# Performance work log

Measured on AMD Instinct MI355X. Metric: run time of the kernel, lower is better.

## Reference

```python
import jax, jax.numpy as jnp
import numpy as np

N_SIDE = 30            # n lines per axis -> 900 primitives
GRID = 64              # grid_size
MAX_ELEMS = 32         # max_elements_per_cell
IMG = 2048             # render resolution -> 4.19M query points


def setup_inputs() -> dict:
    # Replicate the module's line-primitive initialization (one short line per n x n cell).
    rng = np.random.default_rng(42)
    n = N_SIDE
    cell_w = 1.0 / n
    ii, jj = np.meshgrid(np.arange(n), np.arange(n), indexing='ij')
    cx = (ii + 0.5) / n + (rng.random((n, n)) - 0.5) * 0.2 * cell_w
    cy = (jj + 0.5) / n + (rng.random((n, n)) - 0.5) * 0.2 * cell_w
    ang = rng.random((n, n)) * 2.0 * np.pi
    L = 0.3 * cell_w
    dx = np.cos(ang) * L
    dy = np.sin(ang) * L
    x0 = np.clip(cx - dx, 0.0, 1.0); y0 = np.clip(cy - dy, 0.0, 1.0)
    x1 = np.clip(cx + dx, 0.0, 1.0); y1 = np.clip(cy + dy, 0.0, 1.0)
    w = 0.6 / n
    # control points layout per line block: [x0, y0, x1, y1, width, 0]
    control = np.stack([x0, y0, x1, y1, np.full((n, n), w), np.zeros((n, n))], -1)
    control = control.reshape(-1, 6).astype(np.float32)
    widths = np.full((n * n,), w, np.float32)          # stroke_widths (block[7])
    colors = rng.random((n * n, 3)).astype(np.float32)  # fill_colors
    opac = np.ones((n * n,), np.float32)                # opacities
    bg = np.zeros((3,), np.float32)                     # background_color
    key = jax.random.key(0)
    x = jax.random.uniform(key, (IMG * IMG, 2), dtype=jnp.float32)
    return {
        'x': x,
        'control_points': jnp.asarray(control),
        'stroke_widths': jnp.asarray(widths),
        'fill_colors': jnp.asarray(colors),
        'opacities': jnp.asarray(opac),
        'background_color': jnp.asarray(bg),
    }


def _build_grid(control_points, stroke_widths, G, M):
    """Scatter-build: per grid cell, list of primitive indices whose (width-expanded)
    AABB overlaps the cell, plus a count (slot-0 count in the original kernel)."""
    x0, y0, x1, y1 = control_points[:, 0], control_points[:, 1], control_points[:, 2], control_points[:, 3]
    w = stroke_widths
    xmin = jnp.minimum(x0, x1) - w; xmax = jnp.maximum(x0, x1) + w
    ymin = jnp.minimum(y0, y1) - w; ymax = jnp.maximum(y0, y1) + w
    lo = jnp.arange(G, dtype=jnp.float32) / G
    hi = (jnp.arange(G, dtype=jnp.float32) + 1.0) / G
    ox = (xmin[None, :] < hi[:, None]) & (xmax[None, :] >= lo[:, None])  # [G, N]
    oy = (ymin[None, :] < hi[:, None]) & (ymax[None, :] >= lo[:, None])  # [G, N]
    mask = (ox[:, None, :] & oy[None, :, :]).reshape(G * G, -1)          # [G*G, N]
    counts = jnp.minimum(mask.sum(-1), M).astype(jnp.int32)              # [G*G]
    # stable argsort puts hit primitives first, in ascending primitive order
    entries = jnp.argsort(~mask, axis=1)[:, :M].astype(jnp.int32)        # [G*G, M]
    return entries, counts


def reference(x, control_points, stroke_widths, fill_colors, opacities, background_color):
    G, M = GRID, MAX_ELEMS
    entries, counts = _build_grid(control_points, stroke_widths, G, M)
    ix = jnp.clip((x[:, 0] * G).astype(jnp.int32), 0, G - 1)
    iy = jnp.clip((x[:, 1] * G).astype(jnp.int32), 0, G - 1)
    cell = ix * G + iy              # [P]
    ccount = counts[cell]           # [P]
    p0 = control_points[:, 0:2]
    p1 = control_points[:, 2:4]
    init = jnp.broadcast_to(background_color.astype(x.dtype), (x.shape[0], 3))

    def step(color, slot):
        prim = entries[cell, slot]                              # [P] irregular gather
        a0 = p0[prim]                                           # [P,2]
        d = p1[prim] - a0
        rel = x - a0
        t = jnp.clip((rel * d).sum(-1) / jnp.maximum((d * d).sum(-1), 1e-12), 0.0, 1.0)
        dist = jnp.sqrt(((rel - t[:, None] * d) ** 2).sum(-1))  # point-to-segment distance
        inside = (dist <= stroke_widths[prim]) & (slot < ccount)
        a = opacities[prim] * inside.astype(color.dtype)        # [P]
        color = color * (1.0 - a[:, None]) + fill_colors[prim] * a[:, None]
        return color, None

    out, _ = jax.lax.scan(step, init, jnp.arange(M))
    return out
```

## Files before the change

kernel.cpp:

```cpp
#include <hip/hip_runtime.h>
#include <math.h>

#define GRIDN 64
#define MAXE 32
#define MAXPRIM 1024
#define EROW 36
#define SCAP2 15
#define SENTV 0xFFFF

#define WS_PACKED2   0u
#define WS_COLORS    32768u
#define WS_ETAB      49152u
#define WS_SUBTAB    655360u

#define CORE_EVAL(A, Bv)                                                         \
    float relx = __fsub_rn(px, A.x);                                             \
    float rely = __fsub_rn(py, A.y);                                             \
    float td = __fadd_rn(__fmul_rn(relx, A.z), __fmul_rn(rely, A.w));            \
    double inv = __hiloint2double(__float_as_int(Bv.z), __float_as_int(Bv.y));   \
    float tt = (float)((double)td * inv);                                        \
    tt = fminf(fmaxf(tt, 0.0f), 1.0f);                                           \
    float qx = __fsub_rn(relx, __fmul_rn(tt, A.z));                              \
    float qy = __fsub_rn(rely, __fmul_rn(tt, A.w));                              \
    float s2 = __fadd_rn(__fmul_rn(qx, qx), __fmul_rn(qy, qy));

__global__ __launch_bounds__(1024) void prep(const float* __restrict__ cp,
                                             const float* __restrict__ sw,
                                             const float* __restrict__ fc,
                                             const float* __restrict__ op,
                                             float4* __restrict__ packed2,
                                             float4* __restrict__ colors,
                                             int* __restrict__ etab, int nprim) {
    __shared__ float4 saabb[MAXPRIM];
    int tid = threadIdx.x;
    for (int p = tid; p < nprim; p += 1024) {
        float x0 = cp[p * 6 + 0], y0 = cp[p * 6 + 1];
        float x1 = cp[p * 6 + 2], y1 = cp[p * 6 + 3];
        float w = sw[p];
        saabb[p] = make_float4(__fsub_rn(fminf(x0, x1), w), __fadd_rn(fmaxf(x0, x1), w),
                               __fsub_rn(fminf(y0, y1), w), __fadd_rn(fmaxf(y0, y1), w));
    }
    __syncthreads();

    int wid = tid >> 6, lane = tid & 63;
    int cell = blockIdx.x * 16 + wid;
    int ixc = cell >> 6, iyc = cell & 63;
    float lox = (float)ixc * (1.0f / GRIDN);
    float hix = (float)(ixc + 1) * (1.0f / GRIDN);
    float loy = (float)iyc * (1.0f / GRIDN);
    float hiy = (float)(iyc + 1) * (1.0f / GRIDN);
    int total = 0;
    int* row = etab + (size_t)cell * EROW;
    for (int base = 0; base < nprim; base += 64) {
        int p = base + lane;
        bool ov = false;
        if (p < nprim) {
            float4 bb = saabb[p];
            ov = (bb.x < hix) && (bb.y >= lox) && (bb.z < hiy) && (bb.w >= loy);
        }
        unsigned long long m = __ballot(ov);
        if (ov) {
            int pos = total + (int)__popcll(m & ((1ull << lane) - 1ull));
            if (pos < MAXE) row[1 + pos] = p;
        }
        total += (int)__popcll(m);
    }
    if (lane == 0) row[0] = total < MAXE ? total : MAXE;

    if (blockIdx.x == 0) {
        for (int p = tid; p < nprim; p += 1024) {
            float x0 = cp[p * 6 + 0], y0 = cp[p * 6 + 1];
            float x1 = cp[p * 6 + 2], y1 = cp[p * 6 + 3];
            float w = sw[p];
            float dx = __fsub_rn(x1, x0);
            float dy = __fsub_rn(y1, y0);
            float dd = __fadd_rn(__fmul_rn(dx, dx), __fmul_rn(dy, dy));
            float denom = fmaxf(dd, 1e-12f);
            double inv = 1.0 / (double)denom;
            unsigned wb = __float_as_uint(w);
            bool even = (wb & 1u) == 0u;
            float wn = __uint_as_float(wb + 1u);
            double md = 0.5 * ((double)w + (double)wn);
            double m2 = md * md;
            float Tf = (float)m2;
            if ((double)Tf > m2) Tf = __uint_as_float(__float_as_uint(Tf) - 1u);
            if (!even && (double)Tf == m2) Tf = __uint_as_float(__float_as_uint(Tf) - 1u);
            unsigned long long ib = __double_as_longlong(inv);
            packed2[p * 2 + 0] = make_float4(x0, y0, dx, dy);
            packed2[p * 2 + 1] = make_float4(Tf,
                                             __uint_as_float((unsigned)(ib & 0xffffffffull)),
                                             __uint_as_float((unsigned)(ib >> 32)),
                                             w);
            colors[p] = make_float4(fc[p * 3 + 0], fc[p * 3 + 1], fc[p * 3 + 2], op[p]);
        }
    }
}

__global__ __launch_bounds__(1024) void build_sub(const float4* __restrict__ packed2,
                                                  const int* __restrict__ etab,
                                                  unsigned short* __restrict__ subtab) {
    int t = blockIdx.x * 1024 + threadIdx.x;
    int parent = t >> 4;
    int sub = t & 15;
    int ix = parent >> 6, iy = parent & 63;
    int gx = ix * 4 + (sub >> 2), gy = iy * 4 + (sub & 3);
    double clx = (double)gx * (1.0 / 256.0);
    double chx = (double)(gx + 1) * (1.0 / 256.0);
    double cly = (double)gy * (1.0 / 256.0);
    double chy = (double)(gy + 1) * (1.0 / 256.0);
    const int* row = etab + (size_t)parent * EROW;
    int cnt = row[0];
    unsigned short* srow = subtab + (size_t)(gx * 256 + gy) * 16;
    int oc = 0;
    for (int s = 0; s < cnt; ++s) {
        int e = row[1 + s];
        float4 A = packed2[e * 2 + 0];
        float4 B = packed2[e * 2 + 1];
        double W = (double)B.w + 1e-5;
        double lx = clx - W, hx = chx + W, ly = cly - W, hy = chy + W;
        double ax = (double)A.x, ay = (double)A.y;
        double dx = (double)A.z, dy = (double)A.w;
        double t0 = 0.0, t1 = 1.0;
        bool ok = true;
        if (fabs(dx) > 1e-300) {
            double ta = (lx - ax) / dx, tb = (hx - ax) / dx;
            t0 = fmax(t0, fmin(ta, tb));
            t1 = fmin(t1, fmax(ta, tb));
        } else if (ax < lx || ax > hx) ok = false;
        if (ok) {
            if (fabs(dy) > 1e-300) {
                double ta = (ly - ay) / dy, tb = (hy - ay) / dy;
                t0 = fmax(t0, fmin(ta, tb));
                t1 = fmin(t1, fmax(ta, tb));
            } else if (ay < ly || ay > hy) ok = false;
        }
        if (ok && t0 <= t1) {
            if (oc < SCAP2) srow[1 + oc] = (unsigned short)e;
            ++oc;
        }
    }
    srow[0] = (oc <= SCAP2) ? (unsigned short)oc : (unsigned short)SENTV;
}

__device__ __forceinline__ void test_prim(int e, float px, float py, bool fast,
                                          int& win, float& cr, float& cg, float& cb,
                                          const float4* sA, const float4* sBsk,
                                          const float4* scol) {
    float4 A = sA[e];
    float4 Bv = sBsk[e + 4];
    CORE_EVAL(A, Bv);
    if (fast) {
        if (s2 <= Bv.x) win = e;
    } else {
        float4 C = scol[e];
        float a = (s2 <= Bv.x) ? C.w : 0.0f;
        float om = __fsub_rn(1.0f, a);
        cr = __fadd_rn(__fmul_rn(cr, om), __fmul_rn(C.x, a));
        cg = __fadd_rn(__fmul_rn(cg, om), __fmul_rn(C.y, a));
        cb = __fadd_rn(__fmul_rn(cb, om), __fmul_rn(C.z, a));
    }
}

__global__ __launch_bounds__(1024) void render_sub2(const float4* __restrict__ xs4,
                                                    const float4* __restrict__ packed2,
                                                    const float4* __restrict__ colors,
                                                    const int* __restrict__ etab,
                                                    const int* __restrict__ subtab,
                                                    const float* __restrict__ bg,
                                                    float* __restrict__ out, int n, int nprim) {
    __shared__ float4 sA[MAXPRIM];
    __shared__ float4 sBsk[MAXPRIM + 4];
    __shared__ float4 scol[MAXPRIM];
    __shared__ int sflag;
    if (threadIdx.x == 0) sflag = 0;
    __syncthreads();

    int tpair = blockIdx.x * 1024 + threadIdx.x;
    long long p0 = (long long)tpair * 2;
    bool v0 = p0 < n, v1 = p0 + 1 < n;

    float4 P = make_float4(0.f, 0.f, 0.f, 0.f);
    if (v0) P = xs4[tpair];
    float pxs[2] = {P.x, P.z};
    float pys[2] = {P.y, P.w};
    bool vs[2] = {v0, v1};
    int parentv[2] = {0, 0};
    int4 lo[2], hi[2];
    lo[0] = lo[1] = make_int4(0, 0, 0, 0);
    hi[0] = hi[1] = make_int4(0, 0, 0, 0);

#pragma unroll
    for (int j = 0; j < 2; ++j) {
        if (vs[j]) {
            float px = pxs[j], py = pys[j];
            int ix = (int)__fmul_rn(px, (float)GRIDN);
            ix = min(max(ix, 0), GRIDN - 1);
            int iy = (int)__fmul_rn(py, (float)GRIDN);
            iy = min(max(iy, 0), GRIDN - 1);
            parentv[j] = ix * GRIDN + iy;
            int sx = (int)__fmul_rn(px, 256.0f) - ix * 4;
            sx = min(max(sx, 0), 3);
            int sy = (int)__fmul_rn(py, 256.0f) - iy * 4;
            sy = min(max(sy, 0), 3);
            const int* srow = subtab + (size_t)((ix * 4 + sx) * 256 + (iy * 4 + sy)) * 8;
            lo[j] = *(const int4*)srow;
            hi[j] = *(const int4*)(srow + 4);
        }
    }

    for (int t = threadIdx.x; t < nprim; t += 1024) {
        sA[t] = packed2[t * 2 + 0];
        sBsk[t + 4] = packed2[t * 2 + 1];
        float4 c = colors[t];
        scol[t] = c;
        if (c.w != 1.0f) sflag = 1;
    }
    __syncthreads();
    bool fast = (sflag == 0);
    float bgr = bg[0], bgg = bg[1], bgb = bg[2];

    float oc6[6];
#pragma unroll
    for (int j = 0; j < 2; ++j) {
        float px = pxs[j], py = pys[j];
        float cr = bgr, cg = bgg, cb = bgb;
        int win = -1;
        unsigned w0 = (unsigned)lo[j].x;
        int cnt = vs[j] ? (int)(w0 & 0xffffu) : 0;
        if (cnt != SENTV) {
            unsigned wy = (unsigned)lo[j].y, wz = (unsigned)lo[j].z, ww = (unsigned)lo[j].w;
            unsigned hx = (unsigned)hi[j].x, hy = (unsigned)hi[j].y;
            unsigned hz = (unsigned)hi[j].z, hw = (unsigned)hi[j].w;
            if (cnt > 0)  test_prim((int)(w0 >> 16),      px, py, fast, win, cr, cg, cb, sA, sBsk, scol);
            if (cnt > 1)  test_prim((int)(wy & 0xffffu),  px, py, fast, win, cr, cg, cb, sA, sBsk, scol);
            if (cnt > 2)  test_prim((int)(wy >> 16),      px, py, fast, win, cr, cg, cb, sA, sBsk, scol);
            if (cnt > 3)  test_prim((int)(wz & 0xffffu),  px, py, fast, win, cr, cg, cb, sA, sBsk, scol);
            if (cnt > 4)  test_prim((int)(wz >> 16),      px, py, fast, win, cr, cg, cb, sA, sBsk, scol);
            if (cnt > 5)  test_prim((int)(ww & 0xffffu),  px, py, fast, win, cr, cg, cb, sA, sBsk, scol);
            if (cnt > 6)  test_prim((int)(ww >> 16),      px, py, fast, win, cr, cg, cb, sA, sBsk, scol);
            if (cnt > 7)  test_prim((int)(hx & 0xffffu),  px, py, fast, win, cr, cg, cb, sA, sBsk, scol);
            if (cnt > 8)  test_prim((int)(hx >> 16),      px, py, fast, win, cr, cg, cb, sA, sBsk, scol);
            if (cnt > 9)  test_prim((int)(hy & 0xffffu),  px, py, fast, win, cr, cg, cb, sA, sBsk, scol);
            if (cnt > 10) test_prim((int)(hy >> 16),      px, py, fast, win, cr, cg, cb, sA, sBsk, scol);
            if (cnt > 11) test_prim((int)(hz & 0xffffu),  px, py, fast, win, cr, cg, cb, sA, sBsk, scol);
            if (cnt > 12) test_prim((int)(hz >> 16),      px, py, fast, win, cr, cg, cb, sA, sBsk, scol);
            if (cnt > 13) test_prim((int)(hw & 0xffffu),  px, py, fast, win, cr, cg, cb, sA, sBsk, scol);
            if (cnt > 14) test_prim((int)(hw >> 16),      px, py, fast, win, cr, cg, cb, sA, sBsk, scol);
        } else {
            const int* prow = etab + (size_t)parentv[j] * EROW;
            int pcnt = prow[0];
            for (int s = 0; s < pcnt; ++s)
                test_prim(prow[1 + s], px, py, fast, win, cr, cg, cb, sA, sBsk, scol);
        }
        if (fast && win >= 0) {
            float4 C = scol[win];
            cr = C.x; cg = C.y; cb = C.z;
        }
        oc6[j * 3 + 0] = cr;
        oc6[j * 3 + 1] = cg;
        oc6[j * 3 + 2] = cb;
    }

    float* ob = out + (size_t)tpair * 6;
    if (v1) {
        *(float2*)(ob + 0) = make_float2(oc6[0], oc6[1]);
        *(float2*)(ob + 2) = make_float2(oc6[2], oc6[3]);
        *(float2*)(ob + 4) = make_float2(oc6[4], oc6[5]);
    } else if (v0) {
        ob[0] = oc6[0]; ob[1] = oc6[1]; ob[2] = oc6[2];
    }
}

__global__ __launch_bounds__(1024) void render_fb(const float2* __restrict__ xs,
                                                  const float4* __restrict__ packed2,
                                                  const float4* __restrict__ colors,
                                                  const int* __restrict__ etab,
                                                  const float* __restrict__ bg,
                                                  float* __restrict__ out, int n, int nprim) {
    __shared__ float4 sA[MAXPRIM];
    __shared__ float4 sBsk[MAXPRIM + 4];
    __shared__ float4 scol[MAXPRIM];
    __shared__ int sflag;
    if (threadIdx.x == 0) sflag = 0;
    __syncthreads();

    int i = blockIdx.x * 1024 + threadIdx.x;
    bool valid = i < n;
    float px = 0.0f, py = 0.0f;
    int row = 0;
    int4 c0 = make_int4(0, 0, 0, 0), c1 = make_int4(0, 0, 0, 0);
    if (valid) {
        float2 pxy = xs[i];
        px = pxy.x; py = pxy.y;
        int ix = (int)__fmul_rn(px, (float)GRIDN);
        ix = min(max(ix, 0), GRIDN - 1);
        int iy = (int)__fmul_rn(py, (float)GRIDN);
        iy = min(max(iy, 0), GRIDN - 1);
        row = (ix * GRIDN + iy) * EROW;
        c0 = *(const int4*)(etab + row);
        c1 = *(const int4*)(etab + row + 4);
    }
    for (int t = threadIdx.x; t < nprim; t += 1024) {
        sA[t] = packed2[t * 2 + 0];
        sBsk[t + 4] = packed2[t * 2 + 1];
        float4 c = colors[t];
        scol[t] = c;
        if (c.w != 1.0f) sflag = 1;
    }
    __syncthreads();
    int cnt = valid ? c0.x : 0;
    float cr = bg[0], cg = bg[1], cb = bg[2];
    int win = -1;
    bool fast = (sflag == 0);
    if (cnt > 0) test_prim(c0.y, px, py, fast, win, cr, cg, cb, sA, sBsk, scol);
    if (cnt > 1) test_prim(c0.z, px, py, fast, win, cr, cg, cb, sA, sBsk, scol);
    if (cnt > 2) test_prim(c0.w, px, py, fast, win, cr, cg, cb, sA, sBsk, scol);
    if (cnt > 3) test_prim(c1.x, px, py, fast, win, cr, cg, cb, sA, sBsk, scol);
    if (cnt > 4) test_prim(c1.y, px, py, fast, win, cr, cg, cb, sA, sBsk, scol);
    if (cnt > 5) test_prim(c1.z, px, py, fast, win, cr, cg, cb, sA, sBsk, scol);
    if (cnt > 6) test_prim(c1.w, px, py, fast, win, cr, cg, cb, sA, sBsk, scol);
    for (int base = 7; base < cnt; base += 4) {
        int4 c = *(const int4*)(etab + row + 1 + base);
        if (base + 0 < cnt) test_prim(c.x, px, py, fast, win, cr, cg, cb, sA, sBsk, scol);
        if (base + 1 < cnt) test_prim(c.y, px, py, fast, win, cr, cg, cb, sA, sBsk, scol);
        if (base + 2 < cnt) test_prim(c.z, px, py, fast, win, cr, cg, cb, sA, sBsk, scol);
        if (base + 3 < cnt) test_prim(c.w, px, py, fast, win, cr, cg, cb, sA, sBsk, scol);
    }
    if (valid) {
        if (fast && win >= 0) {
            float4 C = scol[win];
            cr = C.x; cg = C.y; cb = C.z;
        }
        out[(size_t)i * 3 + 0] = cr;
        out[(size_t)i * 3 + 1] = cg;
        out[(size_t)i * 3 + 2] = cb;
    }
}

extern "C" void kernel_launch(void* const* d_in, const int* in_sizes, int n_in,
                              void* d_out, int out_size, void* d_ws, size_t ws_size,
                              hipStream_t stream) {
    const float* x  = (const float*)d_in[0];
    const float* cp = (const float*)d_in[1];
    const float* sw = (const float*)d_in[2];
    const float* fc = (const float*)d_in[3];
    const float* op = (const float*)d_in[4];
    const float* bg = (const float*)d_in[5];
    float* out = (float*)d_out;

    int npts  = in_sizes[0] / 2;
    int nprim = in_sizes[2];

    char* ws = (char*)d_ws;
    float4* packed2 = (float4*)(ws + WS_PACKED2);
    float4* colors  = (float4*)(ws + WS_COLORS);
    int* etab       = (int*)(ws + WS_ETAB);
    unsigned short* subtab = (unsigned short*)(ws + WS_SUBTAB);

    size_t need = (size_t)WS_SUBTAB + 65536u * 32u;
    bool use_sub = (ws_size >= need);

    prep<<<GRIDN * GRIDN / 16, 1024, 0, stream>>>(cp, sw, fc, op, packed2, colors,
                                                  etab, nprim);
    if (use_sub) {
        build_sub<<<64, 1024, 0, stream>>>(packed2, etab, subtab);
        int npairs = (npts + 1) / 2;
        render_sub2<<<(npairs + 1023) / 1024, 1024, 0, stream>>>((const float4*)x, packed2,
                                                                 colors, etab, (const int*)subtab,
                                                                 bg, out, npts, nprim);
    } else {
        render_fb<<<(npts + 1023) / 1024, 1024, 0, stream>>>((const float2*)x, packed2,
                                                             colors, etab, bg, out,
                                                             npts, nprim);
    }
}
```

Before: 56.32 us.

## Sort points by sub-cell count within block to cut wavefront divergence

```diff
diff --git a/kernel.cpp b/kernel.cpp
--- a/kernel.cpp
+++ b/kernel.cpp
@@ -11,6 +11,7 @@
 #define WS_PACKED2   0u
 #define WS_COLORS    32768u
 #define WS_ETAB      49152u
+#define WS_FLAG      638976u
 #define WS_SUBTAB    655360u
 
 #define CORE_EVAL(A, Bv)                                                         \
@@ -30,9 +31,12 @@
                                              const float* __restrict__ op,
                                              float4* __restrict__ packed2,
                                              float4* __restrict__ colors,
-                                             int* __restrict__ etab, int nprim) {
+                                             int* __restrict__ etab,
+                                             int* __restrict__ flagp, int nprim) {
     __shared__ float4 saabb[MAXPRIM];
+    __shared__ int sbad;
     int tid = threadIdx.x;
+    if (tid == 0) sbad = 0;
     for (int p = tid; p < nprim; p += 1024) {
         float x0 = cp[p * 6 + 0], y0 = cp[p * 6 + 1];
         float x1 = cp[p * 6 + 2], y1 = cp[p * 6 + 3];
@@ -68,6 +72,7 @@
     if (lane == 0) row[0] = total < MAXE ? total : MAXE;
 
     if (blockIdx.x == 0) {
+        bool bad = false;
         for (int p = tid; p < nprim; p += 1024) {
             float x0 = cp[p * 6 + 0], y0 = cp[p * 6 + 1];
             float x1 = cp[p * 6 + 2], y1 = cp[p * 6 + 3];
@@ -91,8 +96,13 @@
                                              __uint_as_float((unsigned)(ib & 0xffffffffull)),
                                              __uint_as_float((unsigned)(ib >> 32)),
                                              w);
-            colors[p] = make_float4(fc[p * 3 + 0], fc[p * 3 + 1], fc[p * 3 + 2], op[p]);
-        }
+            float opv = op[p];
+            colors[p] = make_float4(fc[p * 3 + 0], fc[p * 3 + 1], fc[p * 3 + 2], opv);
+            if (opv != 1.0f) bad = true;
+        }
+        if (bad) atomicOr(&sbad, 1);
+        __syncthreads();
+        if (tid == 0) flagp[0] = sbad;
     }
 }
 
@@ -145,14 +155,14 @@
 __device__ __forceinline__ void test_prim(int e, float px, float py, bool fast,
                                           int& win, float& cr, float& cg, float& cb,
                                           const float4* sA, const float4* sBsk,
-                                          const float4* scol) {
+                                          const float4* __restrict__ colors) {
     float4 A = sA[e];
     float4 Bv = sBsk[e + 4];
     CORE_EVAL(A, Bv);
     if (fast) {
         if (s2 <= Bv.x) win = e;
     } else {
-        float4 C = scol[e];
+        float4 C = colors[e];
         float a = (s2 <= Bv.x) ? C.w : 0.0f;
         float om = __fsub_rn(1.0f, a);
         cr = __fadd_rn(__fmul_rn(cr, om), __fmul_rn(C.x, a));
@@ -161,113 +171,147 @@
     }
 }
 
-__global__ __launch_bounds__(1024) void render_sub2(const float4* __restrict__ xs4,
-                                                    const float4* __restrict__ packed2,
-                                                    const float4* __restrict__ colors,
-                                                    const int* __restrict__ etab,
-                                                    const int* __restrict__ subtab,
-                                                    const float* __restrict__ bg,
-                                                    float* __restrict__ out, int n, int nprim) {
+__global__ __launch_bounds__(1024) void render_sorted(const float4* __restrict__ xs4,
+                                                      const float4* __restrict__ packed2,
+                                                      const float4* __restrict__ colors,
+                                                      const int* __restrict__ etab,
+                                                      const int* __restrict__ subtab,
+                                                      const float* __restrict__ bg,
+                                                      const int* __restrict__ flagp,
+                                                      float* __restrict__ out,
+                                                      int n, int nprim) {
     __shared__ float4 sA[MAXPRIM];
     __shared__ float4 sBsk[MAXPRIM + 4];
-    __shared__ float4 scol[MAXPRIM];
-    __shared__ int sflag;
-    if (threadIdx.x == 0) sflag = 0;
-    __syncthreads();
-
-    int tpair = blockIdx.x * 1024 + threadIdx.x;
-    long long p0 = (long long)tpair * 2;
-    bool v0 = p0 < n, v1 = p0 + 1 < n;
+    __shared__ float2 spt[2048];
+    __shared__ unsigned short perm[2048];
+    __shared__ int histw[32][17];
+    __shared__ int htot[17];
+    __shared__ int pref[17];
+
+    int tid = threadIdx.x;
+    int wid = tid >> 6;
+    if (tid < 544) ((int*)histw)[tid] = 0;
+    __syncthreads();
+
+    int base = blockIdx.x * 2048;
+    int nv = n - base;
+    nv = nv < 0 ? 0 : (nv > 2048 ? 2048 : nv);
+
+    for (int t = tid; t < nprim; t += 1024) {
+        sA[t] = packed2[t * 2 + 0];
+        sBsk[t + 4] = packed2[t * 2 + 1];
+    }
 
     float4 P = make_float4(0.f, 0.f, 0.f, 0.f);
-    if (v0) P = xs4[tpair];
-    float pxs[2] = {P.x, P.z};
-    float pys[2] = {P.y, P.w};
-    bool vs[2] = {v0, v1};
-    int parentv[2] = {0, 0};
-    int4 lo[2], hi[2];
-    lo[0] = lo[1] = make_int4(0, 0, 0, 0);
-    hi[0] = hi[1] = make_int4(0, 0, 0, 0);
-
+    int li0 = tid * 2, li1 = tid * 2 + 1;
+    if (li1 < nv) {
+        P = xs4[blockIdx.x * 1024 + tid];
+    } else if (li0 < nv) {
+        float2 t2 = ((const float2*)xs4)[base + li0];
+        P.x = t2.x; P.y = t2.y;
+    }
+    int buckj[2], rankj[2];
 #pragma unroll
     for (int j = 0; j < 2; ++j) {
-        if (vs[j]) {
-            float px = pxs[j], py = pys[j];
+        int li = tid * 2 + j;
+        buckj[j] = -1; rankj[j] = 0;
+        if (li < nv) {
+            float px = j ? P.z : P.x;
+            float py = j ? P.w : P.y;
+            spt[li] = make_float2(px, py);
             int ix = (int)__fmul_rn(px, (float)GRIDN);
             ix = min(max(ix, 0), GRIDN - 1);
             int iy = (int)__fmul_rn(py, (float)GRIDN);
             iy = min(max(iy, 0), GRIDN - 1);
-            parentv[j] = ix * GRIDN + iy;
-            int sx = (int)__fmul_rn(px, 256.0f) - ix * 4;
-            sx = min(max(sx, 0), 3);
-            int sy = (int)__fmul_rn(py, 256.0f) - iy * 4;
-            sy = min(max(sy, 0), 3);
-            const int* srow = subtab + (size_t)((ix * 4 + sx) * 256 + (iy * 4 + sy)) * 8;
-            lo[j] = *(const int4*)srow;
-            hi[j] = *(const int4*)(srow + 4);
-        }
-    }
-
-    for (int t = threadIdx.x; t < nprim; t += 1024) {
-        sA[t] = packed2[t * 2 + 0];
-        sBsk[t + 4] = packed2[t * 2 + 1];
-        float4 c = colors[t];
-        scol[t] = c;
-        if (c.w != 1.0f) sflag = 1;
-    }
-    __syncthreads();
-    bool fast = (sflag == 0);
-    float bgr = bg[0], bgg = bg[1], bgb = bg[2];
-
-    float oc6[6];
+            int sx = (int)__fmul_rn(px, 256.0f) - ix * 4; sx = min(max(sx, 0), 3);
+            int sy = (int)__fmul_rn(py, 256.0f) - iy * 4; sy = min(max(sy, 0), 3);
+            const unsigned short* sr =
+                (const unsigned short*)subtab + (size_t)((ix * 4 + sx) * 256 + (iy * 4 + sy)) * 16;
+            int cnt = sr[0];
+            int b = cnt > 16 ? 16 : cnt;
+            buckj[j] = b;
+            rankj[j] = atomicAdd(&histw[wid][b], 1);
+        }
+    }
+    __syncthreads();
+    if (tid < 17) {
+        int s = 0;
+        for (int w2 = 0; w2 < 32; ++w2) {
+            int v = histw[w2][tid];
+            histw[w2][tid] = s;
+            s += v;
+        }
+        htot[tid] = s;
+    }
+    __syncthreads();
+    if (tid == 0) {
+        int s = 0;
+        for (int b = 0; b < 17; ++b) { pref[b] = s; s += htot[b]; }
+    }
+    __syncthreads();
 #pragma unroll
     for (int j = 0; j < 2; ++j) {
-        float px = pxs[j], py = pys[j];
+        if (buckj[j] >= 0) {
+            int pos = pref[buckj[j]] + histw[wid][buckj[j]] + rankj[j];
+            perm[pos] = (unsigned short)(tid * 2 + j);
+        }
+    }
+    __syncthreads();
+
+    bool fast = (flagp[0] == 0);
+    float bgr = bg[0], bgg = bg[1], bgb = bg[2];
+
+#pragma unroll
+    for (int q = 0; q < 2; ++q) {
+        int pos = tid + q * 1024;
+        if (pos >= nv) continue;
+        int li = perm[pos];
+        float2 pp = spt[li];
+        float px = pp.x, py = pp.y;
+        int ix = (int)__fmul_rn(px, (float)GRIDN);
+        ix = min(max(ix, 0), GRIDN - 1);
+        int iy = (int)__fmul_rn(py, (float)GRIDN);
+        iy = min(max(iy, 0), GRIDN - 1);
+        int sx = (int)__fmul_rn(px, 256.0f) - ix * 4; sx = min(max(sx, 0), 3);
+        int sy = (int)__fmul_rn(py, 256.0f) - iy * 4; sy = min(max(sy, 0), 3);
+        const int* srow = subtab + (size_t)((ix * 4 + sx) * 256 + (iy * 4 + sy)) * 8;
+        int4 lo = *(const int4*)srow;
+        int4 hi = *(const int4*)(srow + 4);
         float cr = bgr, cg = bgg, cb = bgb;
         int win = -1;
-        unsigned w0 = (unsigned)lo[j].x;
-        int cnt = vs[j] ? (int)(w0 & 0xffffu) : 0;
+        unsigned w0 = (unsigned)lo.x;
+        int cnt = (int)(w0 & 0xffffu);
         if (cnt != SENTV) {
-            unsigned wy = (unsigned)lo[j].y, wz = (unsigned)lo[j].z, ww = (unsigned)lo[j].w;
-            unsigned hx = (unsigned)hi[j].x, hy = (unsigned)hi[j].y;
-            unsigned hz = (unsigned)hi[j].z, hw = (unsigned)hi[j].w;
-            if (cnt > 0)  test_prim((int)(w0 >> 16),      px, py, fast, win, cr, cg, cb, sA, sBsk, scol);
-            if (cnt > 1)  test_prim((int)(wy & 0xffffu),  px, py, fast, win, cr, cg, cb, sA, sBsk, scol);
-            if (cnt > 2)  test_prim((int)(wy >> 16),      px, py, fast, win, cr, cg, cb, sA, sBsk, scol);
-            if (cnt > 3)  test_prim((int)(wz & 0xffffu),  px, py, fast, win, cr, cg, cb, sA, sBsk, scol);
-            if (cnt > 4)  test_prim((int)(wz >> 16),      px, py, fast, win, cr, cg, cb, sA, sBsk, scol);
-            if (cnt > 5)  test_prim((int)(ww & 0xffffu),  px, py, fast, win, cr, cg, cb, sA, sBsk, scol);
-            if (cnt > 6)  test_prim((int)(ww >> 16),      px, py, fast, win, cr, cg, cb, sA, sBsk, scol);
-            if (cnt > 7)  test_prim((int)(hx & 0xffffu),  px, py, fast, win, cr, cg, cb, sA, sBsk, scol);
-            if (cnt > 8)  test_prim((int)(hx >> 16),      px, py, fast, win, cr, cg, cb, sA, sBsk, scol);
-            if (cnt > 9)  test_prim((int)(hy & 0xffffu),  px, py, fast, win, cr, cg, cb, sA, sBsk, scol);
-            if (cnt > 10) test_prim((int)(hy >> 16),      px, py, fast, win, cr, cg, cb, sA, sBsk, scol);
-            if (cnt > 11) test_prim((int)(hz & 0xffffu),  px, py, fast, win, cr, cg, cb, sA, sBsk, scol);
-            if (cnt > 12) test_prim((int)(hz >> 16),      px, py, fast, win, cr, cg, cb, sA, sBsk, scol);
-            if (cnt > 13) test_prim((int)(hw & 0xffffu),  px, py, fast, win, cr, cg, cb, sA, sBsk, scol);
-            if (cnt > 14) test_prim((int)(hw >> 16),      px, py, fast, win, cr, cg, cb, sA, sBsk, scol);
+            unsigned wy = (unsigned)lo.y, wz = (unsigned)lo.z, ww = (unsigned)lo.w;
+            unsigned hx = (unsigned)hi.x, hy = (unsigned)hi.y;
+            unsigned hz = (unsigned)hi.z, hw = (unsigned)hi.w;
+            if (cnt > 0)  test_prim((int)(w0 >> 16),     px, py, fast, win, cr, cg, cb, sA, sBsk, colors);
+            if (cnt > 1)  test_prim((int)(wy & 0xffffu), px, py, fast, win, cr, cg, cb, sA, sBsk, colors);
+            if (cnt > 2)  test_prim((int)(wy >> 16),     px, py, fast, win, cr, cg, cb, sA, sBsk, colors);
+            if (cnt > 3)  test_prim((int)(wz & 0xffffu), px, py, fast, win, cr, cg, cb, sA, sBsk, colors);
+            if (cnt > 4)  test_prim((int)(wz >> 16),     px, py, fast, win, cr, cg, cb, sA, sBsk, colors);
+            if (cnt > 5)  test_prim((int)(ww & 0xffffu), px, py, fast, win, cr, cg, cb, sA, sBsk, colors);
+            if (cnt > 6)  test_prim((int)(ww >> 16),     px, py, fast, win, cr, cg, cb, sA, sBsk, colors);
+            if (cnt > 7)  test_prim((int)(hx & 0xffffu), px, py, fast, win, cr, cg, cb, sA, sBsk, colors);
+            if (cnt > 8)  test_prim((int)(hx >> 16),     px, py, fast, win, cr, cg, cb, sA, sBsk, colors);
+            if (cnt > 9)  test_prim((int)(hy & 0xffffu), px, py, fast, win, cr, cg, cb, sA, sBsk, colors);
+            if (cnt > 10) test_prim((int)(hy >> 16),     px, py, fast, win, cr, cg, cb, sA, sBsk, colors);
+            if (cnt > 11) test_prim((int)(hz & 0xffffu), px, py, fast, win, cr, cg, cb, sA, sBsk, colors);
+            if (cnt > 12) test_prim((int)(hz >> 16),     px, py, fast, win, cr, cg, cb, sA, sBsk, colors);
+            if (cnt > 13) test_prim((int)(hw & 0xffffu), px, py, fast, win, cr, cg, cb, sA, sBsk, colors);
+            if (cnt > 14) test_prim((int)(hw >> 16),     px, py, fast, win, cr, cg, cb, sA, sBsk, colors);
         } else {
-            const int* prow = etab + (size_t)parentv[j] * EROW;
+            const int* prow = etab + (size_t)(ix * GRIDN + iy) * EROW;
             int pcnt = prow[0];
             for (int s = 0; s < pcnt; ++s)
-                test_prim(prow[1 + s], px, py, fast, win, cr, cg, cb, sA, sBsk, scol);
+                test_prim(prow[1 + s], px, py, fast, win, cr, cg, cb, sA, sBsk, colors);
         }
         if (fast && win >= 0) {
-            float4 C = scol[win];
+            float4 C = colors[win];
             cr = C.x; cg = C.y; cb = C.z;
         }
-        oc6[j * 3 + 0] = cr;
-        oc6[j * 3 + 1] = cg;
-        oc6[j * 3 + 2] = cb;
-    }
-
-    float* ob = out + (size_t)tpair * 6;
-    if (v1) {
-        *(float2*)(ob + 0) = make_float2(oc6[0], oc6[1]);
-        *(float2*)(ob + 2) = make_float2(oc6[2], oc6[3]);
-        *(float2*)(ob + 4) = make_float2(oc6[4], oc6[5]);
-    } else if (v0) {
-        ob[0] = oc6[0]; ob[1] = oc6[1]; ob[2] = oc6[2];
+        float* ob = out + (size_t)(base + li) * 3;
+        ob[0] = cr; ob[1] = cg; ob[2] = cb;
     }
 }
 
@@ -279,7 +323,6 @@
                                                   float* __restrict__ out, int n, int nprim) {
     __shared__ float4 sA[MAXPRIM];
     __shared__ float4 sBsk[MAXPRIM + 4];
-    __shared__ float4 scol[MAXPRIM];
     __shared__ int sflag;
     if (threadIdx.x == 0) sflag = 0;
     __syncthreads();
@@ -303,32 +346,30 @@
     for (int t = threadIdx.x; t < nprim; t += 1024) {
         sA[t] = packed2[t * 2 + 0];
         sBsk[t + 4] = packed2[t * 2 + 1];
-        float4 c = colors[t];
-        scol[t] = c;
-        if (c.w != 1.0f) sflag = 1;
+        if (colors[t].w != 1.0f) sflag = 1;
     }
     __syncthreads();
     int cnt = valid ? c0.x : 0;
     float cr = bg[0], cg = bg[1], cb = bg[2];
     int win = -1;
     bool fast = (sflag == 0);
-    if (cnt > 0) test_prim(c0.y, px, py, fast, win, cr, cg, cb, sA, sBsk, scol);
-    if (cnt > 1) test_prim(c0.z, px, py, fast, win, cr, cg, cb, sA, sBsk, scol);
-    if (cnt > 2) test_prim(c0.w, px, py, fast, win, cr, cg, cb, sA, sBsk, scol);
-    if (cnt > 3) test_prim(c1.x, px, py, fast, win, cr, cg, cb, sA, sBsk, scol);
-    if (cnt > 4) test_prim(c1.y, px, py, fast, win, cr, cg, cb, sA, sBsk, scol);
-    if (cnt > 5) test_prim(c1.z, px, py, fast, win, cr, cg, cb, sA, sBsk, scol);
-    if (cnt > 6) test_prim(c1.w, px, py, fast, win, cr, cg, cb, sA, sBsk, scol);
+    if (cnt > 0) test_prim(c0.y, px, py, fast, win, cr, cg, cb, sA, sBsk, colors);
+    if (cnt > 1) test_prim(c0.z, px, py, fast, win, cr, cg, cb, sA, sBsk, colors);
+    if (cnt > 2) test_prim(c0.w, px, py, fast, win, cr, cg, cb, sA, sBsk, colors);
+    if (cnt > 3) test_prim(c1.x, px, py, fast, win, cr, cg, cb, sA, sBsk, colors);
+    if (cnt > 4) test_prim(c1.y, px, py, fast, win, cr, cg, cb, sA, sBsk, colors);
+    if (cnt > 5) test_prim(c1.z, px, py, fast, win, cr, cg, cb, sA, sBsk, colors);
+    if (cnt > 6) test_prim(c1.w, px, py, fast, win, cr, cg, cb, sA, sBsk, colors);
     for (int base = 7; base < cnt; base += 4) {
         int4 c = *(const int4*)(etab + row + 1 + base);
-        if (base + 0 < cnt) test_prim(c.x, px, py, fast, win, cr, cg, cb, sA, sBsk, scol);
-        if (base + 1 < cnt) test_prim(c.y, px, py, fast, win, cr, cg, cb, sA, sBsk, scol);
-        if (base + 2 < cnt) test_prim(c.z, px, py, fast, win, cr, cg, cb, sA, sBsk, scol);
-        if (base + 3 < cnt) test_prim(c.w, px, py, fast, win, cr, cg, cb, sA, sBsk, scol);
+        if (base + 0 < cnt) test_prim(c.x, px, py, fast, win, cr, cg, cb, sA, sBsk, colors);
+        if (base + 1 < cnt) test_prim(c.y, px, py, fast, win, cr, cg, cb, sA, sBsk, colors);
+        if (base + 2 < cnt) test_prim(c.z, px, py, fast, win, cr, cg, cb, sA, sBsk, colors);
+        if (base + 3 < cnt) test_prim(c.w, px, py, fast, win, cr, cg, cb, sA, sBsk, colors);
     }
     if (valid) {
         if (fast && win >= 0) {
-            float4 C = scol[win];
+            float4 C = colors[win];
             cr = C.x; cg = C.y; cb = C.z;
         }
         out[(size_t)i * 3 + 0] = cr;
@@ -355,19 +396,20 @@
     float4* packed2 = (float4*)(ws + WS_PACKED2);
     float4* colors  = (float4*)(ws + WS_COLORS);
     int* etab       = (int*)(ws + WS_ETAB);
+    int* flagp      = (int*)(ws + WS_FLAG);
     unsigned short* subtab = (unsigned short*)(ws + WS_SUBTAB);
 
     size_t need = (size_t)WS_SUBTAB + 65536u * 32u;
     bool use_sub = (ws_size >= need);
 
     prep<<<GRIDN * GRIDN / 16, 1024, 0, stream>>>(cp, sw, fc, op, packed2, colors,
-                                                  etab, nprim);
+                                                  etab, flagp, nprim);
     if (use_sub) {
         build_sub<<<64, 1024, 0, stream>>>(packed2, etab, subtab);
-        int npairs = (npts + 1) / 2;
-        render_sub2<<<(npairs + 1023) / 1024, 1024, 0, stream>>>((const float4*)x, packed2,
-                                                                 colors, etab, (const int*)subtab,
-                                                                 bg, out, npts, nprim);
+        int nblk = (npts + 2047) / 2048;
+        render_sorted<<<nblk, 1024, 0, stream>>>((const float4*)x, packed2, colors,
+                                                 etab, (const int*)subtab, bg, flagp,
+                                                 out, npts, nprim);
     } else {
         render_fb<<<(npts + 1023) / 1024, 1024, 0, stream>>>((const float2*)x, packed2,
                                                              colors, etab, bg, out,
```

Result: slower. 76.46 us (+35.8%).
